# Optimization experiments

Measured on AMD Instinct MI355X. Metric: run time of the kernel, lower is better.

The kernel has to match this reference:

```python
import jax, jax.numpy as jnp
import numpy as np

EPS = 1e-5

def setup_inputs() -> dict:
    key = jax.random.key(0)
    ks = jax.random.split(key, 6)
    C, r = 64, 4
    x = jax.random.normal(ks[0], (2, C, 16, 16, 16), dtype=jnp.float32)
    # ConvTranspose3d(C, C, kernel=r, stride=r, groups=C): weight [C, 1, r, r, r] -> squeeze to [C, r, r, r]
    w_ct = jax.random.normal(ks[1], (C, r, r, r), dtype=jnp.float32) * (1.0 / np.sqrt(r**3))
    b_ct = jax.random.normal(ks[2], (C,), dtype=jnp.float32) * 0.02
    # GroupNorm(num_groups=1) affine params
    gamma = jnp.ones((C,), dtype=jnp.float32)
    beta = jnp.zeros((C,), dtype=jnp.float32)
    # Conv3d(C, C, kernel=1, bias=False): weight [C, C, 1, 1, 1] -> [C_out, C_in]
    w_pw = jax.random.normal(ks[3], (C, C), dtype=jnp.float32) * (1.0 / np.sqrt(C))
    return {"x": x, "w_ct": w_ct, "b_ct": b_ct, "gamma": gamma, "beta": beta, "w_pw": w_pw}

def reference(x, w_ct, b_ct, gamma, beta, w_pw):
    N, C, D, H, W = x.shape
    r = w_ct.shape[-1]
    # Depthwise ConvTranspose3d with kernel==stride: non-overlapping scatter-multiply.
    # out[n,c,d*r+i,h*r+j,w*r+k] = x[n,c,d,h,w] * w_ct[c,i,j,k] + b_ct[c]
    y = jnp.einsum('ncdhw,cijk->ncdihjwk', x, w_ct).reshape(N, C, D * r, H * r, W * r)
    y = y + b_ct[None, :, None, None, None]
    # GroupNorm(num_groups=1): normalize over (C, D, H, W) per sample, per-channel affine.
    mean = jnp.mean(y, axis=(1, 2, 3, 4), keepdims=True)
    var = jnp.mean(jnp.square(y - mean), axis=(1, 2, 3, 4), keepdims=True)
    yn = (y - mean) * jax.lax.rsqrt(var + EPS)
    yn = yn * gamma[None, :, None, None, None] + beta[None, :, None, None, None]
    # Pointwise 1x1x1 conv (no bias): channel-mixing GEMM.
    out = jnp.einsum('ncdhw,oc->nodhw', yn, w_pw)
    return out
```

## Files before the change

kernel.cpp:

```cpp
#include <hip/hip_runtime.h>

typedef unsigned short u16;
typedef __attribute__((ext_vector_type(8))) short s16x8;
typedef __attribute__((ext_vector_type(4))) float f32x4;
typedef __attribute__((ext_vector_type(4))) unsigned int u32x4;

__device__ __forceinline__ u16 f2bf(float f) {
    unsigned u = __builtin_bit_cast(unsigned, f);
    u += 0x7fffu + ((u >> 16) & 1u);
    return (u16)(u >> 16);
}
__device__ __forceinline__ float lo_bf(unsigned v) {
    return __builtin_bit_cast(float, v << 16);
}
__device__ __forceinline__ float hi_bf(unsigned v) {
    return __builtin_bit_cast(float, v & 0xffff0000u);
}

#define WS_SX   0
#define WS_SX2  128

__global__ __launch_bounds__(256) void k_reduce(const float* __restrict__ x,
                                                float* __restrict__ ws) {
    int nc = blockIdx.x;
    const f32x4* p = (const f32x4*)(x + (size_t)nc * 4096);
    int t = threadIdx.x;
    float s = 0.f, s2 = 0.f;
    for (int it = 0; it < 4; ++it) {
        f32x4 v = p[t + it * 256];
        for (int e = 0; e < 4; ++e) { s += v[e]; s2 += v[e] * v[e]; }
    }
    for (int off = 32; off; off >>= 1) {
        s  += __shfl_down(s, off);
        s2 += __shfl_down(s2, off);
    }
    __shared__ float rs[4], rs2[4];
    int lane = t & 63, wv = t >> 6;
    if (lane == 0) { rs[wv] = s; rs2[wv] = s2; }
    __syncthreads();
    if (t == 0) {
        ws[WS_SX  + nc] = rs[0] + rs[1] + rs[2] + rs[3];
        ws[WS_SX2 + nc] = rs2[0] + rs2[1] + rs2[2] + rs2[3];
    }
}

#define SWS 96
#define STG_LD 260
__global__ __launch_bounds__(256, 2) void k_main(const float* __restrict__ x,
                                              const float* __restrict__ w_ct,
                                              const float* __restrict__ b_ct,
                                              const float* __restrict__ gamma,
                                              const float* __restrict__ beta,
                                              const float* __restrict__ w_pw,
                                              const float* __restrict__ ws,
                                              float* __restrict__ out) {
    __shared__ __align__(16) u16   sWb[64 * SWS];
    __shared__ __align__(16) u16   sXb[64 * SWS];
    __shared__ __align__(16) float sA[64 * 68];
    __shared__ float sK[64];
    __shared__ float p_sw[256], p_sw2[256];
    __shared__ float s_b[64], s_g[64], s_be[64];
    __shared__ float s_mi[2];
    __shared__ __align__(16) float stg[32 * STG_LD];

    int t = threadIdx.x;
    int B = blockIdx.x;
    int b = (B & 7) * 64 + (B >> 3);
    int n = b >> 8, dd = (b >> 2) & 63, hq = b & 3;
    int d = dd >> 2, i_f = dd & 3;

    {
        int c = t & 63, qr = t >> 6;
        const f32x4* wp = (const f32x4*)(w_ct + c * 64 + qr * 16);
        float sw = 0.f, sw2 = 0.f;
        for (int r = 0; r < 4; ++r) {
            f32x4 v = wp[r];
            for (int e = 0; e < 4; ++e) {
                float f = v[e];
                sw += f; sw2 += f * f;
                sWb[(qr * 16 + r * 4 + e) * SWS + c] = f2bf(f);
            }
        }
        p_sw[t] = sw; p_sw2[t] = sw2;
    }
    {
        int c = t & 63, h_loc = t >> 6;
        const f32x4* xp = (const f32x4*)(x + ((size_t)n * 64 + c) * 4096
                                           + d * 256 + (hq * 4 + h_loc) * 16);
        for (int r = 0; r < 4; ++r) {
            f32x4 v = xp[r];
            for (int e = 0; e < 4; ++e)
                sXb[(h_loc * 16 + r * 4 + e) * SWS + c] = f2bf(v[e]);
        }
    }
    if (t < 64) { s_b[t] = b_ct[t]; s_g[t] = gamma[t]; s_be[t] = beta[t]; }
    __syncthreads();

    if (t < 64) {
        int c = t;
        float sw  = p_sw[c]  + p_sw[64 + c]  + p_sw[128 + c]  + p_sw[192 + c];
        float sw2 = p_sw2[c] + p_sw2[64 + c] + p_sw2[128 + c] + p_sw2[192 + c];
        float sx  = ws[WS_SX  + n * 64 + c];
        float sx2 = ws[WS_SX2 + n * 64 + c];
        float bc  = s_b[c];
        float ty  = sw  * sx  + 262144.f * bc;
        float ty2 = sw2 * sx2 + 2.f * bc * sw * sx + 262144.f * bc * bc;
        for (int off = 32; off; off >>= 1) {
            ty  += __shfl_down(ty, off);
            ty2 += __shfl_down(ty2, off);
        }
        if (t == 0) {
            float mean = ty * (1.f / 16777216.f);
            float var  = ty2 * (1.f / 16777216.f) - mean * mean;
            s_mi[0] = mean;
            s_mi[1] = rsqrtf(var + 1e-5f);
        }
    }
    __syncthreads();

    float mean = s_mi[0], inv = s_mi[1];
    for (int k = 0; k < 16; ++k) {
        int idx = t + k * 256;
        int c = idx & 63;
        sA[(idx >> 6) * 68 + c] = w_pw[idx] * s_g[c] * inv;
    }
    if (t < 64) {
        int o = t;
        const f32x4* wp = (const f32x4*)(w_pw + o * 64);
        float k = 0.f;
        for (int r = 0; r < 16; ++r) {
            f32x4 v = wp[r];
            for (int e = 0; e < 4; ++e) {
                int c = r * 4 + e;
                k += v[e] * (s_g[c] * inv * (s_b[c] - mean) + s_be[c]);
            }
        }
        sK[o] = k;
    }
    __syncthreads();

    int lane = t & 63;
    int wid  = t >> 6;
    int colq = lane & 15;
    int quad = lane >> 4;

    s16x8 afrag[4][2];
    for (int mt = 0; mt < 4; ++mt) {
        int o = mt * 16 + colq;
        for (int kt = 0; kt < 2; ++kt) {
            int c0 = kt * 32 + quad * 8;
            const float* ap = &sA[o * 68 + c0];
            f32x4 f0 = *(const f32x4*)ap;
            f32x4 f1 = *(const f32x4*)(ap + 4);
            s16x8 fr;
            fr[0] = (short)f2bf(f0[0]); fr[1] = (short)f2bf(f0[1]);
            fr[2] = (short)f2bf(f0[2]); fr[3] = (short)f2bf(f0[3]);
            fr[4] = (short)f2bf(f1[0]); fr[5] = (short)f2bf(f1[1]);
            fr[6] = (short)f2bf(f1[2]); fr[7] = (short)f2bf(f1[3]);
            afrag[mt][kt] = fr;
        }
    }
    f32x4 kinit[4];
    for (int mt = 0; mt < 4; ++mt) {
        float kv = sK[mt * 16 + colq];
        kinit[mt][0] = kv; kinit[mt][1] = kv; kinit[mt][2] = kv; kinit[mt][3] = kv;
    }

    size_t base_n = (size_t)n << 24;

    for (int s = 0; s < 4; ++s) {
        f32x4 acc[4][4];

        #pragma unroll
        for (int tt = 0; tt < 4; ++tt) {
            int Woff = tt * 16 + colq;
            int wi   = Woff >> 2;
            int kf   = Woff & 3;
            int ijk  = i_f * 16 + wid * 4 + kf;
            int xrow = s * 16 + wi;

            s16x8 bfrag[2];
            #pragma unroll
            for (int kt = 0; kt < 2; ++kt) {
                int c0 = kt * 32 + quad * 8;
                u32x4 wv = *(const u32x4*)&sWb[ijk  * SWS + c0];
                u32x4 xv = *(const u32x4*)&sXb[xrow * SWS + c0];
                s16x8 fr;
                for (int e = 0; e < 4; ++e) {
                    float pl = lo_bf(wv[e]) * lo_bf(xv[e]);
                    float ph = hi_bf(wv[e]) * hi_bf(xv[e]);
                    fr[2 * e]     = (short)f2bf(pl);
                    fr[2 * e + 1] = (short)f2bf(ph);
                }
                bfrag[kt] = fr;
            }
            #pragma unroll
            for (int mt = 0; mt < 4; ++mt) {
                f32x4 a = kinit[mt];
                a = __builtin_amdgcn_mfma_f32_16x16x32_bf16(bfrag[0], afrag[mt][0], a, 0, 0, 0);
                a = __builtin_amdgcn_mfma_f32_16x16x32_bf16(bfrag[1], afrag[mt][1], a, 0, 0, 0);
                acc[tt][mt] = a;
            }
        }

        #pragma unroll
        for (int ho = 0; ho < 2; ++ho) {
            #pragma unroll
            for (int tt = 0; tt < 4; ++tt) {
                #pragma unroll
                for (int m2 = 0; m2 < 2; ++m2) {
                    int o_loc = m2 * 16 + colq;
                    int q_loc = wid * 64 + tt * 16 + quad * 4;
                    *(f32x4*)&stg[o_loc * STG_LD + q_loc] = acc[tt][ho * 2 + m2];
                }
            }
            __syncthreads();
            size_t gb = base_n + (size_t)(dd * 4096 + hq * 1024 + s * 256 + lane * 4);
            #pragma unroll
            for (int it = 0; it < 8; ++it) {
                int o = ho * 32 + it * 4 + wid;
                f32x4 v = *(const f32x4*)&stg[(o & 31) * STG_LD + lane * 4];
                *(f32x4*)(out + gb + ((size_t)o << 18)) = v;
            }
            __syncthreads();
        }
    }
}

extern "C" void kernel_launch(void* const* d_in, const int* in_sizes, int n_in,
                              void* d_out, int out_size, void* d_ws, size_t ws_size,
                              hipStream_t stream) {
    const float* x     = (const float*)d_in[0];
    const float* w_ct  = (const float*)d_in[1];
    const float* b_ct  = (const float*)d_in[2];
    const float* gamma = (const float*)d_in[3];
    const float* beta  = (const float*)d_in[4];
    const float* w_pw  = (const float*)d_in[5];
    float* ws  = (float*)d_ws;
    float* out = (float*)d_out;

    k_reduce<<<128, 256, 0, stream>>>(x, ws);
    k_main<<<512, 256, 0, stream>>>(x, w_ct, b_ct, gamma, beta, w_pw, ws, out);
}
```

Before: 152.3 us.

## Restructure output staging per 16-channel group with contiguous 4KB row stores

Reorders the main loop so each pass handles one 16-output-channel M tile across all four spatial slices. Results are staged in a larger shared buffer that aliases the no-longer-needed sA array, then written as contiguous 4KB runs per output channel. The aim is longer sequential global writes and fewer barrier rounds per tile. In exchange, shared memory per block grows, and launch bounds drop to one block per SM, which lowers occupancy and may leave the MFMA and store phases less overlapped.

```diff
diff --git a/kernel.cpp b/kernel.cpp
--- a/kernel.cpp
+++ b/kernel.cpp
@@ -45,8 +45,8 @@
 }
 
 #define SWS 96
-#define STG_LD 260
-__global__ __launch_bounds__(256, 2) void k_main(const float* __restrict__ x,
+#define STG_LD 1028
+__global__ __launch_bounds__(256, 1) void k_main(const float* __restrict__ x,
                                               const float* __restrict__ w_ct,
                                               const float* __restrict__ b_ct,
                                               const float* __restrict__ gamma,
@@ -56,12 +56,13 @@
                                               float* __restrict__ out) {
     __shared__ __align__(16) u16   sWb[64 * SWS];
     __shared__ __align__(16) u16   sXb[64 * SWS];
-    __shared__ __align__(16) float sA[64 * 68];
+    __shared__ __align__(16) float stg[16 * STG_LD];
     __shared__ float sK[64];
     __shared__ float p_sw[256], p_sw2[256];
     __shared__ float s_b[64], s_g[64], s_be[64];
     __shared__ float s_mi[2];
-    __shared__ __align__(16) float stg[32 * STG_LD];
+
+    float* sA = stg;
 
     int t = threadIdx.x;
     int B = blockIdx.x;
@@ -165,65 +166,59 @@
         float kv = sK[mt * 16 + colq];
         kinit[mt][0] = kv; kinit[mt][1] = kv; kinit[mt][2] = kv; kinit[mt][3] = kv;
     }
+    __syncthreads();
 
     size_t base_n = (size_t)n << 24;
-
-    for (int s = 0; s < 4; ++s) {
-        f32x4 acc[4][4];
-
+    size_t rgn    = (size_t)(dd * 4096 + hq * 1024);
+
+    for (int p = 0; p < 4; ++p) {
         #pragma unroll
-        for (int tt = 0; tt < 4; ++tt) {
-            int Woff = tt * 16 + colq;
-            int wi   = Woff >> 2;
-            int kf   = Woff & 3;
-            int ijk  = i_f * 16 + wid * 4 + kf;
-            int xrow = s * 16 + wi;
-
-            s16x8 bfrag[2];
-            #pragma unroll
-            for (int kt = 0; kt < 2; ++kt) {
-                int c0 = kt * 32 + quad * 8;
-                u32x4 wv = *(const u32x4*)&sWb[ijk  * SWS + c0];
-                u32x4 xv = *(const u32x4*)&sXb[xrow * SWS + c0];
-                s16x8 fr;
-                for (int e = 0; e < 4; ++e) {
-                    float pl = lo_bf(wv[e]) * lo_bf(xv[e]);
-                    float ph = hi_bf(wv[e]) * hi_bf(xv[e]);
-                    fr[2 * e]     = (short)f2bf(pl);
-                    fr[2 * e + 1] = (short)f2bf(ph);
-                }
-                bfrag[kt] = fr;
-            }
-            #pragma unroll
-            for (int mt = 0; mt < 4; ++mt) {
-                f32x4 a = kinit[mt];
-                a = __builtin_amdgcn_mfma_f32_16x16x32_bf16(bfrag[0], afrag[mt][0], a, 0, 0, 0);
-                a = __builtin_amdgcn_mfma_f32_16x16x32_bf16(bfrag[1], afrag[mt][1], a, 0, 0, 0);
-                acc[tt][mt] = a;
-            }
-        }
-
-        #pragma unroll
-        for (int ho = 0; ho < 2; ++ho) {
+        for (int s = 0; s < 4; ++s) {
             #pragma unroll
             for (int tt = 0; tt < 4; ++tt) {
+                int Woff = tt * 16 + colq;
+                int wi   = Woff >> 2;
+                int kf   = Woff & 3;
+                int ijk  = i_f * 16 + wid * 4 + kf;
+                int xrow = s * 16 + wi;
+
+                s16x8 bfrag[2];
                 #pragma unroll
-                for (int m2 = 0; m2 < 2; ++m2) {
-                    int o_loc = m2 * 16 + colq;
-                    int q_loc = wid * 64 + tt * 16 + quad * 4;
-                    *(f32x4*)&stg[o_loc * STG_LD + q_loc] = acc[tt][ho * 2 + m2];
+                for (int kt = 0; kt < 2; ++kt) {
+                    int c0 = kt * 32 + quad * 8;
+                    u32x4 wv = *(const u32x4*)&sWb[ijk  * SWS + c0];
+                    u32x4 xv = *(const u32x4*)&sXb[xrow * SWS + c0];
+                    s16x8 fr;
+                    for (int e = 0; e < 4; ++e) {
+                        float pl = lo_bf(wv[e]) * lo_bf(xv[e]);
+                        float ph = hi_bf(wv[e]) * hi_bf(xv[e]);
+                        fr[2 * e]     = (short)f2bf(pl);
+                        fr[2 * e + 1] = (short)f2bf(ph);
+                    }
+                    bfrag[kt] = fr;
                 }
-            }
-            __syncthreads();
-            size_t gb = base_n + (size_t)(dd * 4096 + hq * 1024 + s * 256 + lane * 4);
+                f32x4 a = kinit[p];
+                a = __builtin_amdgcn_mfma_f32_16x16x32_bf16(bfrag[0], afrag[p][0], a, 0, 0, 0);
+                a = __builtin_amdgcn_mfma_f32_16x16x32_bf16(bfrag[1], afrag[p][1], a, 0, 0, 0);
+                int q_loc = s * 256 + wid * 64 + tt * 16 + quad * 4;
+                *(f32x4*)&stg[colq * STG_LD + q_loc] = a;
+            }
+        }
+        __syncthreads();
+
+        #pragma unroll
+        for (int oo = 0; oo < 4; ++oo) {
+            int o_loc = wid * 4 + oo;
+            int o     = p * 16 + o_loc;
+            const float* src = &stg[o_loc * STG_LD + lane * 4];
+            float* dst = out + base_n + ((size_t)o << 18) + rgn + lane * 4;
             #pragma unroll
-            for (int it = 0; it < 8; ++it) {
-                int o = ho * 32 + it * 4 + wid;
-                f32x4 v = *(const f32x4*)&stg[(o & 31) * STG_LD + lane * 4];
-                *(f32x4*)(out + gb + ((size_t)o << 18)) = v;
-            }
-            __syncthreads();
-        }
+            for (int k = 0; k < 4; ++k) {
+                f32x4 v = *(const f32x4*)(src + k * 256);
+                *(f32x4*)(dst + k * 256) = v;
+            }
+        }
+        __syncthreads();
     }
 }
 
```

New measurement: 230.6 us. 1.51x slower.
